# Performance work log

Hardware: AMD Instinct MI355X
Metric: run time of the kernel (lower is better)

## Reference

```python
import jax, jax.numpy as jnp
import numpy as np

EPSILON = 1e-8
MAX_WEIGHT = 0.15
N_ITER = 20
STEP_SIZE = 0.05
B, P = 32768, 45


def _simplex_projection(w):
    # clamp + renormalize, done twice (differentiable approximation)
    w = jnp.clip(w, 0.0, MAX_WEIGHT)
    w = w / (jnp.sum(w, axis=-1, keepdims=True) + EPSILON)
    w = jnp.clip(w, 0.0, MAX_WEIGHT)
    w = w / (jnp.sum(w, axis=-1, keepdims=True) + EPSILON)
    return w


def setup_inputs() -> dict:
    key = jax.random.key(0)
    k1, k2 = jax.random.split(key, 2)
    # SPD-ish covariance for a well-behaved iterative solve
    A = jax.random.normal(k1, (B, P, P), dtype=jnp.float32) * 0.1
    sigma = jnp.einsum('bij,bkj->bik', A, A) + 0.1 * jnp.eye(P, dtype=jnp.float32)
    beta = jax.nn.softmax(jax.random.normal(k2, (B, P), dtype=jnp.float32), axis=-1)
    w_prev = jnp.full((B, P), 1.0 / P, dtype=jnp.float32)
    return {
        'sigma': sigma,
        'beta': beta,
        'w_prev': w_prev,
        'log_lambda_sparse': jnp.asarray(-3.0, dtype=jnp.float32),
        'log_lambda_turnover': jnp.asarray(-2.0, dtype=jnp.float32),
    }


def reference(sigma, beta, w_prev, log_lambda_sparse, log_lambda_turnover):
    Bb, Pp = beta.shape
    lam_s = jnp.exp(log_lambda_sparse)
    lam_t = jnp.exp(log_lambda_turnover)
    w0 = jnp.full((Bb, Pp), 1.0 / Pp, dtype=sigma.dtype)

    def step(w, _):
        Sw = jnp.einsum('bij,bj->bi', sigma, w)  # [B,P]
        grad = 2.0 * Sw - beta + lam_s * jnp.sign(w) + 2.0 * lam_t * (w - w_prev)
        w = _simplex_projection(w - STEP_SIZE * grad)
        return w, None

    w, _ = jax.lax.scan(step, w0, None, length=N_ITER)
    return w
```

## Files before the change

kernel.cpp:

```cpp
#include <hip/hip_runtime.h>
#include <math.h>

#define P 45
#define N_ITER 20

__global__ __launch_bounds__(64) void drb_kernel(
    const float* __restrict__ sigma,
    const float* __restrict__ beta,
    const float* __restrict__ w_prev,
    const float* __restrict__ lls,
    const float* __restrict__ llt,
    float* __restrict__ out)
{
    const int b    = blockIdx.x;
    const int lane = threadIdx.x;

    const float lam_s  = expf(lls[0]);
    const float lam_t2 = 2.0f * expf(llt[0]);

    const size_t base = (size_t)b * (P * P);

    float row[P];
    float bet = 0.0f, wp = 0.0f, wc = 0.0f;
    if (lane < P) {
        const float* rp = sigma + base + (size_t)lane * P;
        #pragma unroll
        for (int j = 0; j < P; ++j) row[j] = rp[j];
        bet = beta[(size_t)b * P + lane];
        wp  = w_prev[(size_t)b * P + lane];
        wc  = (float)(1.0 / 45.0);
    } else {
        #pragma unroll
        for (int j = 0; j < P; ++j) row[j] = 0.0f;
    }

    __shared__ __align__(16) float w_sh[P];
    if (lane < P) w_sh[lane] = wc;
    __syncthreads();

    for (int it = 0; it < N_ITER; ++it) {
        float wv[P];
        #pragma unroll
        for (int j = 0; j < P; ++j) wv[j] = w_sh[j];

        float acc = 0.0f;
        #pragma unroll
        for (int j = 0; j < P; ++j) acc = fmaf(row[j], wv[j], acc);

        float sgn = (wc > 0.0f) ? 1.0f : ((wc < 0.0f) ? -1.0f : 0.0f);
        float g   = 2.0f * acc - bet + lam_s * sgn + lam_t2 * (wc - wp);
        float wn  = wc - 0.05f * g;

        wn = fminf(fmaxf(wn, 0.0f), 0.15f);
        float s = wn;
        #pragma unroll
        for (int m = 1; m < 64; m <<= 1) s += __shfl_xor(s, m, 64);
        wn = wn / (s + 1e-8f);

        wn = fminf(fmaxf(wn, 0.0f), 0.15f);
        float s2 = wn;
        #pragma unroll
        for (int m = 1; m < 64; m <<= 1) s2 += __shfl_xor(s2, m, 64);
        wn = wn / (s2 + 1e-8f);

        wc = wn;

        __syncthreads();
        if (lane < P) w_sh[lane] = wc;
        __syncthreads();
    }

    if (lane < P) out[(size_t)b * P + lane] = wc;
}

extern "C" void kernel_launch(void* const* d_in, const int* in_sizes, int n_in,
                              void* d_out, int out_size, void* d_ws, size_t ws_size,
                              hipStream_t stream) {
    const float* sigma  = (const float*)d_in[0];
    const float* beta   = (const float*)d_in[1];
    const float* w_prev = (const float*)d_in[2];
    const float* lls    = (const float*)d_in[3];
    const float* llt    = (const float*)d_in[4];
    float* out = (float*)d_out;

    const int B = in_sizes[1] / P;
    drb_kernel<<<B, 64, 0, stream>>>(sigma, beta, w_prev, lls, llt, out);
}
```

Before: 416.4 us.

## Replace shared-memory weight exchange with readlane broadcasts and DPP wave reductions

Removes the shared-memory buffer and both block barriers per iteration. Each lane now reads the weight vector directly from other lanes via readlane, splits the dot product across two accumulators, and replaces the shuffle-based sum with DPP row operations plus a final readlane. Division is swapped for a hardware reciprocal multiply, which is slightly less precise. Inactive lanes load a clamped row so the loads are unconditional, and an empty asm statement keeps the row values in registers. The dominant cost is likely the 8 KB per-block sigma load, so the loop savings may matter less.

```diff
diff --git a/kernel.cpp b/kernel.cpp
--- a/kernel.cpp
+++ b/kernel.cpp
@@ -3,6 +3,24 @@
 
 #define P 45
 #define N_ITER 20
+
+template<int CTRL>
+__device__ __forceinline__ float dpp_add(float x) {
+    int xi = __builtin_bit_cast(int, x);
+    int yi = __builtin_amdgcn_update_dpp(0, xi, CTRL, 0xF, 0xF, true);
+    return x + __builtin_bit_cast(float, yi);
+}
+
+__device__ __forceinline__ float wave_sum_bcast(float x) {
+    x = dpp_add<0x111>(x);
+    x = dpp_add<0x112>(x);
+    x = dpp_add<0x114>(x);
+    x = dpp_add<0x118>(x);
+    x = dpp_add<0x142>(x);
+    x = dpp_add<0x143>(x);
+    int si = __builtin_amdgcn_readlane(__builtin_bit_cast(int, x), 63);
+    return __builtin_bit_cast(float, si);
+}
 
 __global__ __launch_bounds__(64) void drb_kernel(
     const float* __restrict__ sigma,
@@ -14,63 +32,56 @@
 {
     const int b    = blockIdx.x;
     const int lane = threadIdx.x;
+    const bool active = lane < P;
+    const int  r   = active ? lane : (P - 1);
 
     const float lam_s  = expf(lls[0]);
     const float lam_t2 = 2.0f * expf(llt[0]);
 
-    const size_t base = (size_t)b * (P * P);
+    const float* rp = sigma + (size_t)b * (P * P) + (size_t)r * P;
+    float row[P];
+    #pragma unroll
+    for (int j = 0; j < P; ++j) row[j] = rp[j];
+    #pragma unroll
+    for (int j = 0; j < P; ++j) asm volatile("" : "+v"(row[j]));
 
-    float row[P];
-    float bet = 0.0f, wp = 0.0f, wc = 0.0f;
-    if (lane < P) {
-        const float* rp = sigma + base + (size_t)lane * P;
-        #pragma unroll
-        for (int j = 0; j < P; ++j) row[j] = rp[j];
-        bet = beta[(size_t)b * P + lane];
-        wp  = w_prev[(size_t)b * P + lane];
-        wc  = (float)(1.0 / 45.0);
-    } else {
-        #pragma unroll
-        for (int j = 0; j < P; ++j) row[j] = 0.0f;
-    }
-
-    __shared__ __align__(16) float w_sh[P];
-    if (lane < P) w_sh[lane] = wc;
-    __syncthreads();
+    float bet = active ? beta[(size_t)b * P + lane]   : 0.0f;
+    float wp  = active ? w_prev[(size_t)b * P + lane] : 0.0f;
+    float wc  = active ? (float)(1.0 / 45.0)          : 0.0f;
 
     for (int it = 0; it < N_ITER; ++it) {
-        float wv[P];
+        const int wci = __builtin_bit_cast(int, wc);
+        float acc0 = 0.0f, acc1 = 0.0f;
         #pragma unroll
-        for (int j = 0; j < P; ++j) wv[j] = w_sh[j];
-
-        float acc = 0.0f;
-        #pragma unroll
-        for (int j = 0; j < P; ++j) acc = fmaf(row[j], wv[j], acc);
+        for (int j = 0; j + 1 < P; j += 2) {
+            float w0 = __builtin_bit_cast(float, __builtin_amdgcn_readlane(wci, j));
+            float w1 = __builtin_bit_cast(float, __builtin_amdgcn_readlane(wci, j + 1));
+            acc0 = fmaf(row[j],     w0, acc0);
+            acc1 = fmaf(row[j + 1], w1, acc1);
+        }
+        {
+            float w44 = __builtin_bit_cast(float, __builtin_amdgcn_readlane(wci, P - 1));
+            acc0 = fmaf(row[P - 1], w44, acc0);
+        }
+        const float acc = acc0 + acc1;
 
         float sgn = (wc > 0.0f) ? 1.0f : ((wc < 0.0f) ? -1.0f : 0.0f);
         float g   = 2.0f * acc - bet + lam_s * sgn + lam_t2 * (wc - wp);
         float wn  = wc - 0.05f * g;
+        wn = active ? wn : 0.0f;
 
         wn = fminf(fmaxf(wn, 0.0f), 0.15f);
-        float s = wn;
-        #pragma unroll
-        for (int m = 1; m < 64; m <<= 1) s += __shfl_xor(s, m, 64);
-        wn = wn / (s + 1e-8f);
+        float s   = wave_sum_bcast(wn);
+        wn *= __builtin_amdgcn_rcpf(s + 1e-8f);
 
         wn = fminf(fmaxf(wn, 0.0f), 0.15f);
-        float s2 = wn;
-        #pragma unroll
-        for (int m = 1; m < 64; m <<= 1) s2 += __shfl_xor(s2, m, 64);
-        wn = wn / (s2 + 1e-8f);
+        s   = wave_sum_bcast(wn);
+        wn *= __builtin_amdgcn_rcpf(s + 1e-8f);
 
         wc = wn;
-
-        __syncthreads();
-        if (lane < P) w_sh[lane] = wc;
-        __syncthreads();
     }
 
-    if (lane < P) out[(size_t)b * P + lane] = wc;
+    if (active) out[(size_t)b * P + lane] = wc;
 }
 
 extern "C" void kernel_launch(void* const* d_in, const int* in_sizes, int n_in,
```

New measurement: 394.4 us. 5.3% less time.
